# Kernel optimization log

Measured on AMD Instinct MI355X. Metric: run time of the kernel, lower is better.

The kernel has to match this reference:

```python
import jax, jax.numpy as jnp
import numpy as np

D_IN, N_HEADS, N_KV, HEAD_DIM = 2048, 8, 4, 256
GROUP = N_HEADS // N_KV
SCALING = 256.0 ** -0.5  # query_pre_attn_scalar = 256
EPS = 1e-6


def _rms_norm(x, gamma):
    # Gemma-style RMSNorm with (1 + gamma) scale, over last dim (head_dim)
    var = jnp.mean(x * x, axis=-1, keepdims=True)
    return x * jax.lax.rsqrt(var + EPS) * (1.0 + gamma)


def _apply_rope(x, cos, sin):
    # x: [b, h, s, d]; cos/sin: [s, d] (rotate-half convention)
    d = x.shape[-1]
    x1, x2 = x[..., : d // 2], x[..., d // 2:]
    rotated = jnp.concatenate([-x2, x1], axis=-1)
    return x * cos[None, None] + rotated * sin[None, None]


def setup_inputs() -> dict:
    key = jax.random.key(0)
    ks = jax.random.split(key, 6)
    b, s = 2, 2048
    x = jax.random.normal(ks[0], (b, s, D_IN), dtype=jnp.float32)
    # causal mask: True above diagonal = masked
    mask = jnp.triu(jnp.ones((s, s), dtype=bool), k=1)
    # RoPE tables (base 10000)
    inv_freq = 1.0 / (10000.0 ** (jnp.arange(0, HEAD_DIM, 2, dtype=jnp.float32) / HEAD_DIM))
    angles = jnp.arange(s, dtype=jnp.float32)[:, None] * inv_freq[None, :]  # [s, d/2]
    angles = jnp.concatenate([angles, angles], axis=-1)  # [s, d]
    cos, sin = jnp.cos(angles), jnp.sin(angles)
    std = 0.02
    wq = jax.random.normal(ks[1], (N_HEADS * HEAD_DIM, D_IN), dtype=jnp.float32) * std
    wk = jax.random.normal(ks[2], (N_KV * HEAD_DIM, D_IN), dtype=jnp.float32) * std
    wv = jax.random.normal(ks[3], (N_KV * HEAD_DIM, D_IN), dtype=jnp.float32) * std
    wo = jax.random.normal(ks[4], (D_IN, N_HEADS * HEAD_DIM), dtype=jnp.float32) * std
    q_gamma = jnp.zeros((HEAD_DIM,), dtype=jnp.float32)
    k_gamma = jnp.zeros((HEAD_DIM,), dtype=jnp.float32)
    return {"x": x, "mask": mask, "cos": cos, "sin": sin,
            "wq": wq, "wk": wk, "wv": wv, "wo": wo,
            "q_gamma": q_gamma, "k_gamma": k_gamma}


def reference(x, mask, cos, sin, wq, wk, wv, wo, q_gamma, k_gamma):
    b, s, _ = x.shape
    # projections (torch Linear: y = x @ W.T)
    q = (x @ wq.T).reshape(b, s, N_HEADS, HEAD_DIM).transpose(0, 2, 1, 3)  # [b,H,s,d]
    k = (x @ wk.T).reshape(b, s, N_KV, HEAD_DIM).transpose(0, 2, 1, 3)     # [b,G,s,d]
    v = (x @ wv.T).reshape(b, s, N_KV, HEAD_DIM).transpose(0, 2, 1, 3)     # [b,G,s,d]
    q = _rms_norm(q, q_gamma)
    k = _rms_norm(k, k_gamma)
    q = _apply_rope(q, cos, sin) * SCALING
    k = _apply_rope(k, cos, sin)
    # GQA via broadcast (avoids repeat_interleave): head h = g*GROUP + j (group-major)
    qg = q.reshape(b, N_KV, GROUP, s, HEAD_DIM)
    scores = jnp.einsum('bgjqd,bgkd->bgjqk', qg, k)  # [b,G,group,s,s]
    scores = jnp.where(mask[None, None, None], -jnp.inf, scores)
    weights = jax.nn.softmax(scores, axis=-1)
    ctx = jnp.einsum('bgjqk,bgkd->bgjqd', weights, v)  # [b,G,group,s,d]
    ctx = ctx.reshape(b, N_HEADS, s, HEAD_DIM).transpose(0, 2, 1, 3).reshape(b, s, N_HEADS * HEAD_DIM)
    return ctx @ wo.T
```

## Files before the change

### kernel.cpp

```cpp
#include <hip/hip_runtime.h>
#include <math.h>


typedef __bf16 bf16x8 __attribute__((ext_vector_type(8)));
typedef __bf16 bf16x4 __attribute__((ext_vector_type(4)));
typedef float  f32x4  __attribute__((ext_vector_type(4)));

#define MFMA16(a, b, c) __builtin_amdgcn_mfma_f32_16x16x32_bf16(a, b, c, 0, 0, 0)

__device__ __forceinline__ void async16(const __bf16* g, const __bf16* l) {
  __builtin_amdgcn_global_load_lds(
      (__attribute__((address_space(1))) const void*)g,
      (__attribute__((address_space(3))) void*)l, 16, 0, 0);
}

__global__ __launch_bounds__(256) void cast_f32_bf16(
    const float* __restrict__ src, __bf16* __restrict__ dst) {
  const size_t i = ((size_t)blockIdx.x * 256 + threadIdx.x) * 4;
  f32x4 v = *(const f32x4*)(src + i);
  bf16x4 o;
#pragma unroll
  for (int j = 0; j < 4; j++) o[j] = (__bf16)v[j];
  *(bf16x4*)(dst + i) = o;
}

template <typename OT>
__device__ __forceinline__ void gemm_body(const __bf16* A, const __bf16* B,
                                          OT* C, size_t m0, size_t n0,
                                          size_t ccol0, int ldc) {
  constexpr int K = 2048;
  __shared__ __align__(16) __bf16 As[128 * 32];
  __shared__ __align__(16) __bf16 Bs[128 * 32];
  const int tid = threadIdx.x;
  const int wave = tid >> 6, lane = tid & 63;
  const int lr = lane & 15, lq = lane >> 4;
  const int wm = (wave >> 1) * 64, wn = (wave & 1) * 64;

  f32x4 acc[4][4];
#pragma unroll
  for (int i = 0; i < 4; i++)
#pragma unroll
    for (int j = 0; j < 4; j++)
#pragma unroll
      for (int r = 0; r < 4; r++) acc[i][j][r] = 0.f;

  int srow[2], skof[2];
#pragma unroll
  for (int c = 0; c < 2; c++) {
    const int t = wave * 2 + c;
    const int g = t * 8 + (lane >> 3);
    const int cc = (lane & 7) ^ (g & 7);
    srow[c] = g * 2 + (cc >> 2);
    skof[c] = (cc & 3) * 8;
  }

  for (int k0 = 0; k0 < K; k0 += 32) {
#pragma unroll
    for (int c = 0; c < 2; c++) {
      const int t = wave * 2 + c;
      async16(A + (m0 + srow[c]) * K + k0 + skof[c], As + t * 512);
      async16(B + (n0 + srow[c]) * K + k0 + skof[c], Bs + t * 512);
    }
    __syncthreads();
    bf16x8 af[4], bf[4];
#pragma unroll
    for (int i = 0; i < 4; i++) {
      const int row = wm + i * 16 + lr;
      const int g = row >> 1;
      const int p = ((row & 1) * 4 + lq) ^ (g & 7);
      af[i] = *(const bf16x8*)&As[g * 64 + p * 8];
    }
#pragma unroll
    for (int j = 0; j < 4; j++) {
      const int row = wn + j * 16 + lr;
      const int g = row >> 1;
      const int p = ((row & 1) * 4 + lq) ^ (g & 7);
      bf[j] = *(const bf16x8*)&Bs[g * 64 + p * 8];
    }
#pragma unroll
    for (int i = 0; i < 4; i++)
#pragma unroll
      for (int j = 0; j < 4; j++)
        acc[i][j] = MFMA16(af[i], bf[j], acc[i][j]);
    __syncthreads();
  }

#pragma unroll
  for (int i = 0; i < 4; i++)
#pragma unroll
    for (int j = 0; j < 4; j++)
#pragma unroll
      for (int r = 0; r < 4; r++) {
        const size_t row = m0 + wm + i * 16 + lq * 4 + r;
        const size_t col = ccol0 + wn + j * 16 + lr;
        C[row * (size_t)ldc + col] = (OT)acc[i][j][r];
      }
}

template <typename OT>
__global__ __launch_bounds__(256) void gemm_bt(
    const __bf16* __restrict__ A, const __bf16* __restrict__ B,
    OT* __restrict__ C, const int ldc) {
  gemm_body<OT>(A, B, C, (size_t)blockIdx.y * 128, (size_t)blockIdx.x * 128,
                (size_t)blockIdx.x * 128, ldc);
}

__global__ __launch_bounds__(256) void gemm_qkv(
    const __bf16* __restrict__ A, const __bf16* __restrict__ Bq,
    const __bf16* __restrict__ Bk, const __bf16* __restrict__ Bv,
    __bf16* __restrict__ C) {
  const int bx = blockIdx.x;
  const __bf16* B;
  int nl;
  if (bx < 16) { B = Bq; nl = bx; }
  else if (bx < 24) { B = Bk; nl = bx - 16; }
  else { B = Bv; nl = bx - 24; }
  gemm_body<__bf16>(A, B, C, (size_t)blockIdx.y * 128, (size_t)nl * 128,
                    (size_t)bx * 128, 4096);
}

__global__ __launch_bounds__(256) void rmsrope(
    const __bf16* __restrict__ qkv, const float* __restrict__ cosb,
    const float* __restrict__ sinb, const float* __restrict__ qg,
    const float* __restrict__ kg, __bf16* __restrict__ qrot,
    __bf16* __restrict__ krot) {
  const int wave = threadIdx.x >> 6, lane = threadIdx.x & 63;
  const int rid = blockIdx.x * 4 + wave;
  const int m = rid / 12, seg = rid % 12;
  const int b = m >> 11, pos = m & 2047;
  const bool isq = seg < 8;
  const int col = isq ? seg * 256 : 2048 + (seg - 8) * 256;
  const int d = lane * 4;

  bf16x4 xv = *(const bf16x4*)(qkv + (size_t)m * 4096 + col + d);
  float x[4];
#pragma unroll
  for (int i = 0; i < 4; i++) x[i] = (float)xv[i];
  float ss = x[0] * x[0] + x[1] * x[1] + x[2] * x[2] + x[3] * x[3];
#pragma unroll
  for (int off = 1; off < 64; off <<= 1) ss += __shfl_xor(ss, off);
  const float inv = rsqrtf(ss * (1.f / 256.f) + 1e-6f);

  f32x4 gv = *(const f32x4*)((isq ? qg : kg) + d);
  float xn[4];
#pragma unroll
  for (int i = 0; i < 4; i++) xn[i] = x[i] * inv * (1.f + gv[i]);
  float rot[4];
#pragma unroll
  for (int i = 0; i < 4; i++) {
    const float pn = __shfl_xor(xn[i], 32);
    rot[i] = (lane < 32) ? -pn : pn;
  }
  f32x4 cv = *(const f32x4*)(cosb + (size_t)pos * 256 + d);
  f32x4 sv = *(const f32x4*)(sinb + (size_t)pos * 256 + d);
  const float sc = isq ? 0.0625f : 1.f;
  bf16x4 ov;
#pragma unroll
  for (int i = 0; i < 4; i++)
    ov[i] = (__bf16)((xn[i] * cv[i] + rot[i] * sv[i]) * sc);
  __bf16* dst = isq
      ? qrot + ((size_t)(b * 8 + seg) * 2048 + pos) * 256 + d
      : krot + ((size_t)(b * 4 + (seg - 8)) * 2048 + pos) * 256 + d;
  *(bf16x4*)dst = ov;
}

__global__ __launch_bounds__(256) void vtrans(const __bf16* __restrict__ qkv,
                                              __bf16* __restrict__ vT) {
  __shared__ __bf16 tile[64 * 65];
  const int bkv = blockIdx.z;
  const int d0 = blockIdx.y * 64, p0 = blockIdx.x * 64;
  const int t = threadIdx.x;
  const int b = bkv >> 2, kv = bkv & 3;
#pragma unroll
  for (int i = 0; i < 16; i++) {
    const int f = i * 256 + t;
    const int pl = f >> 6, dl = f & 63;
    tile[pl * 65 + dl] =
        qkv[(size_t)(b * 2048 + p0 + pl) * 4096 + 3072 + kv * 256 + d0 + dl];
  }
  __syncthreads();
#pragma unroll
  for (int i = 0; i < 16; i++) {
    const int f = i * 256 + t;
    const int dl = f >> 6, pl = f & 63;
    vT[((size_t)bkv * 256 + d0 + dl) * 2048 + p0 + pl] = tile[pl * 65 + dl];
  }
}

__global__ __launch_bounds__(128) void flash(
    const __bf16* __restrict__ qrot, const __bf16* __restrict__ krot,
    const __bf16* __restrict__ vT, __bf16* __restrict__ ctx) {
  __shared__ __align__(16) __bf16 Ks[64 * 256];
  __shared__ __align__(16) __bf16 Vs[256 * 64];
  __shared__ __align__(16) __bf16 Ps[2 * 32 * 64];
  const int tid = threadIdx.x, wave = tid >> 6, lane = tid & 63;
  const int lr = lane & 15, lq = lane >> 4;
  const int qt = (int)gridDim.x - 1 - (int)blockIdx.x;
  const int h = blockIdx.y, b = blockIdx.z, kv = h >> 1;
  const int q0 = qt * 64 + wave * 32;

  bf16x8 qf[2][8];
  {
    const __bf16* qbb = qrot + (size_t)(b * 8 + h) * 2048 * 256;
#pragma unroll
    for (int qi = 0; qi < 2; qi++)
#pragma unroll
      for (int i = 0; i < 8; i++)
        qf[qi][i] = *(const bf16x8*)(qbb + (size_t)(q0 + qi * 16 + lr) * 256 +
                                     i * 32 + lq * 8);
  }
  f32x4 acc[2][16];
#pragma unroll
  for (int qi = 0; qi < 2; qi++)
#pragma unroll
    for (int j = 0; j < 16; j++)
#pragma unroll
      for (int r = 0; r < 4; r++) acc[qi][j][r] = 0.f;
  float lsum[2][4];
#pragma unroll
  for (int qi = 0; qi < 2; qi++)
#pragma unroll
    for (int r = 0; r < 4; r++) lsum[qi][r] = 0.f;

  const __bf16* kbase = krot + (size_t)(b * 4 + kv) * 2048 * 256;
  const __bf16* vbase = vT + (size_t)(b * 4 + kv) * 256 * 2048;

  int koff[16], voff[16];
#pragma unroll
  for (int c = 0; c < 16; c++) {
    const int t = wave * 16 + c;
    {
      const int row = t * 2 + (lane >> 5);
      const int ch = (lane & 31) ^ (row & 31);
      koff[c] = row * 256 + ch * 8;
    }
    {
      const int d = t * 8 + (lane >> 3);
      const int ch = (lane & 7) ^ (d & 7);
      voff[c] = d * 2048 + ch * 8;
    }
  }

  for (int kt = 0; kt <= qt; kt++) {
    const int k0 = kt * 64;
#pragma unroll
    for (int c = 0; c < 16; c++) {
      const int t = wave * 16 + c;
      async16(kbase + (size_t)k0 * 256 + koff[c], Ks + t * 512);
      async16(vbase + k0 + voff[c], Vs + t * 512);
    }
    __syncthreads();

    f32x4 s[2][4];
#pragma unroll
    for (int qi = 0; qi < 2; qi++)
#pragma unroll
      for (int f = 0; f < 4; f++)
#pragma unroll
        for (int r = 0; r < 4; r++) s[qi][f][r] = 0.f;
#pragma unroll
    for (int i = 0; i < 8; i++) {
      bf16x8 kf[4];
#pragma unroll
      for (int f = 0; f < 4; f++) {
        const int row = f * 16 + lr;
        const int pch = (i * 4 + lq) ^ (row & 31);
        kf[f] = *(const bf16x8*)&Ks[row * 256 + pch * 8];
      }
#pragma unroll
      for (int qi = 0; qi < 2; qi++)
#pragma unroll
        for (int f = 0; f < 4; f++)
          s[qi][f] = MFMA16(qf[qi][i], kf[f], s[qi][f]);
    }

    const bool diag = (kt == qt);
#pragma unroll
    for (int qi = 0; qi < 2; qi++) {
      const int qa = q0 + qi * 16 + lq * 4;
#pragma unroll
      for (int f = 0; f < 4; f++) {
        const int ka = k0 + f * 16 + lr;
        const int row = qi * 16 + lq * 4;
        const int pchb = (f * 2 + (lr >> 3));
#pragma unroll
        for (int r = 0; r < 4; r++) {
          float p = __expf(s[qi][f][r] - 16.f);
          if (diag && ka > qa + r) p = 0.f;
          lsum[qi][r] += p;
          Ps[wave * 2048 + (row + r) * 64 + (pchb ^ ((row + r) & 7)) * 8 +
             (lr & 7)] = (__bf16)p;
        }
      }
    }
    asm volatile("s_waitcnt lgkmcnt(0)" ::: "memory");

#pragma unroll
    for (int m = 0; m < 2; m++) {
      bf16x8 pf[2];
#pragma unroll
      for (int qi = 0; qi < 2; qi++) {
        const int row = qi * 16 + lr;
        const int pch = (m * 4 + lq) ^ (row & 7);
        pf[qi] = *(const bf16x8*)&Ps[wave * 2048 + row * 64 + pch * 8];
      }
#pragma unroll
      for (int j = 0; j < 16; j++) {
        const int d = j * 16 + lr;
        const int pch = (m * 4 + lq) ^ (d & 7);
        bf16x8 vf = *(const bf16x8*)&Vs[d * 64 + pch * 8];
#pragma unroll
        for (int qi = 0; qi < 2; qi++)
          acc[qi][j] = MFMA16(pf[qi], vf, acc[qi][j]);
      }
    }
    __syncthreads();
  }

  float inv[2][4];
#pragma unroll
  for (int qi = 0; qi < 2; qi++)
#pragma unroll
    for (int r = 0; r < 4; r++) {
      float l = lsum[qi][r];
#pragma unroll
      for (int off = 1; off < 16; off <<= 1) l += __shfl_xor(l, off);
      inv[qi][r] = 1.f / l;
    }
#pragma unroll
  for (int qi = 0; qi < 2; qi++)
#pragma unroll
    for (int j = 0; j < 16; j++)
#pragma unroll
      for (int r = 0; r < 4; r++) {
        const int row = q0 + qi * 16 + lq * 4 + r;
        ctx[((size_t)(b * 2048 + row) * 8 + h) * 256 + j * 16 + lr] =
            (__bf16)(acc[qi][j][r] * inv[qi][r]);
      }
}

extern "C" void kernel_launch(void* const* d_in, const int* in_sizes, int n_in,
                              void* d_out, int out_size, void* d_ws,
                              size_t ws_size, hipStream_t stream) {
  const float* x = (const float*)d_in[0];
  const float* cosb = (const float*)d_in[2];
  const float* sinb = (const float*)d_in[3];
  const float* wq = (const float*)d_in[4];
  const float* wk = (const float*)d_in[5];
  const float* wv = (const float*)d_in[6];
  const float* wo = (const float*)d_in[7];
  const float* qg = (const float*)d_in[8];
  const float* kg = (const float*)d_in[9];
  float* out = (float*)d_out;

  char* ws = (char*)d_ws;
  __bf16* xbf = (__bf16*)ws;
  __bf16* wqbf = (__bf16*)(ws + ((size_t)16 << 20));
  __bf16* wkbf = (__bf16*)(ws + ((size_t)24 << 20));
  __bf16* wvbf = (__bf16*)(ws + ((size_t)28 << 20));
  __bf16* qkv = (__bf16*)(ws + ((size_t)32 << 20));
  __bf16* qrot = (__bf16*)ws;
  __bf16* krot = (__bf16*)(ws + ((size_t)16 << 20));
  __bf16* vTp = (__bf16*)(ws + ((size_t)24 << 20));
  __bf16* wobf = (__bf16*)(ws + ((size_t)32 << 20));
  __bf16* ctx = (__bf16*)(ws + ((size_t)40 << 20));

  cast_f32_bf16<<<8192, 256, 0, stream>>>(x, xbf);
  cast_f32_bf16<<<4096, 256, 0, stream>>>(wq, wqbf);
  cast_f32_bf16<<<2048, 256, 0, stream>>>(wk, wkbf);
  cast_f32_bf16<<<2048, 256, 0, stream>>>(wv, wvbf);

  gemm_qkv<<<dim3(32, 32), 256, 0, stream>>>(xbf, wqbf, wkbf, wvbf, qkv);

  rmsrope<<<12288, 256, 0, stream>>>(qkv, cosb, sinb, qg, kg, qrot, krot);
  vtrans<<<dim3(32, 4, 8), 256, 0, stream>>>(qkv, vTp);

  cast_f32_bf16<<<4096, 256, 0, stream>>>(wo, wobf);
  flash<<<dim3(32, 8, 2), 128, 0, stream>>>(qrot, krot, vTp, ctx);

  gemm_bt<float><<<dim3(16, 32), 256, 0, stream>>>(ctx, wobf, out, 2048);
}
```

Baseline: 425.2 us.

## Double-buffer K/V tiles in flash kernel and use 4-wave 128-query blocks

```diff
diff --git a/kernel.cpp b/kernel.cpp
--- a/kernel.cpp
+++ b/kernel.cpp
@@ -187,17 +187,17 @@
   }
 }
 
-__global__ __launch_bounds__(128) void flash(
+__global__ __launch_bounds__(256) void flash(
     const __bf16* __restrict__ qrot, const __bf16* __restrict__ krot,
     const __bf16* __restrict__ vT, __bf16* __restrict__ ctx) {
-  __shared__ __align__(16) __bf16 Ks[64 * 256];
-  __shared__ __align__(16) __bf16 Vs[256 * 64];
-  __shared__ __align__(16) __bf16 Ps[2 * 32 * 64];
+  __shared__ __align__(16) __bf16 Ks[2][64 * 256];
+  __shared__ __align__(16) __bf16 Vs[2][256 * 64];
+  __shared__ __align__(16) __bf16 Ps[4 * 32 * 64];
   const int tid = threadIdx.x, wave = tid >> 6, lane = tid & 63;
   const int lr = lane & 15, lq = lane >> 4;
-  const int qt = (int)gridDim.x - 1 - (int)blockIdx.x;
+  const int Q = blockIdx.x;
   const int h = blockIdx.y, b = blockIdx.z, kv = h >> 1;
-  const int q0 = qt * 64 + wave * 32;
+  const int q0 = Q * 128 + wave * 32;
 
   bf16x8 qf[2][8];
   {
@@ -225,10 +225,10 @@
   const __bf16* kbase = krot + (size_t)(b * 4 + kv) * 2048 * 256;
   const __bf16* vbase = vT + (size_t)(b * 4 + kv) * 256 * 2048;
 
-  int koff[16], voff[16];
-#pragma unroll
-  for (int c = 0; c < 16; c++) {
-    const int t = wave * 16 + c;
+  int koff[8], voff[8];
+#pragma unroll
+  for (int c = 0; c < 8; c++) {
+    const int t = wave * 8 + c;
     {
       const int row = t * 2 + (lane >> 5);
       const int ch = (lane & 31) ^ (row & 31);
@@ -241,15 +241,30 @@
     }
   }
 
-  for (int kt = 0; kt <= qt; kt++) {
+  const int nt = 2 * Q + 2;
+
+#define STAGE(kt_, buf_)                                                   \
+  {                                                                        \
+    const int k0_ = (kt_)*64;                                              \
+    _Pragma("unroll") for (int c = 0; c < 8; c++) {                        \
+      const int t = wave * 8 + c;                                          \
+      async16(kbase + (size_t)k0_ * 256 + koff[c], Ks[buf_] + t * 512);    \
+      async16(vbase + k0_ + voff[c], Vs[buf_] + t * 512);                  \
+    }                                                                      \
+  }
+
+  STAGE(0, 0);
+
+  for (int kt = 0; kt < nt; kt++) {
+    const int cur = kt & 1;
     const int k0 = kt * 64;
-#pragma unroll
-    for (int c = 0; c < 16; c++) {
-      const int t = wave * 16 + c;
-      async16(kbase + (size_t)k0 * 256 + koff[c], Ks + t * 512);
-      async16(vbase + k0 + voff[c], Vs + t * 512);
-    }
-    __syncthreads();
+    if (kt + 1 < nt) {
+      STAGE(kt + 1, cur ^ 1);
+      asm volatile("s_waitcnt vmcnt(16)" ::: "memory");
+    } else {
+      asm volatile("s_waitcnt vmcnt(0)" ::: "memory");
+    }
+    __builtin_amdgcn_s_barrier();
 
     f32x4 s[2][4];
 #pragma unroll
@@ -265,7 +280,7 @@
       for (int f = 0; f < 4; f++) {
         const int row = f * 16 + lr;
         const int pch = (i * 4 + lq) ^ (row & 31);
-        kf[f] = *(const bf16x8*)&Ks[row * 256 + pch * 8];
+        kf[f] = *(const bf16x8*)&Ks[cur][row * 256 + pch * 8];
       }
 #pragma unroll
       for (int qi = 0; qi < 2; qi++)
@@ -274,7 +289,7 @@
           s[qi][f] = MFMA16(qf[qi][i], kf[f], s[qi][f]);
     }
 
-    const bool diag = (kt == qt);
+    const bool diag = (k0 + 63 > q0);
 #pragma unroll
     for (int qi = 0; qi < 2; qi++) {
       const int qa = q0 + qi * 16 + lq * 4;
@@ -308,14 +323,15 @@
       for (int j = 0; j < 16; j++) {
         const int d = j * 16 + lr;
         const int pch = (m * 4 + lq) ^ (d & 7);
-        bf16x8 vf = *(const bf16x8*)&Vs[d * 64 + pch * 8];
+        bf16x8 vf = *(const bf16x8*)&Vs[cur][d * 64 + pch * 8];
 #pragma unroll
         for (int qi = 0; qi < 2; qi++)
           acc[qi][j] = MFMA16(pf[qi], vf, acc[qi][j]);
       }
     }
-    __syncthreads();
-  }
+    __builtin_amdgcn_s_barrier();
+  }
+#undef STAGE
 
   float inv[2][4];
 #pragma unroll
@@ -376,7 +392,7 @@
   vtrans<<<dim3(32, 4, 8), 256, 0, stream>>>(qkv, vTp);
 
   cast_f32_bf16<<<4096, 256, 0, stream>>>(wo, wobf);
-  flash<<<dim3(32, 8, 2), 128, 0, stream>>>(qrot, krot, vTp, ctx);
+  flash<<<dim3(16, 8, 2), 256, 0, stream>>>(qrot, krot, vTp, ctx);
 
   gemm_bt<float><<<dim3(16, 32), 256, 0, stream>>>(ctx, wobf, out, 2048);
 }
```

Result: no change. 425.8 us (+0.1%).

## Use 256x256-tile 8-wave QKV GEMM with double-buffered async LDS loads

Applied to the files above, without the earlier changes.

```diff
diff --git a/kernel.cpp b/kernel.cpp
--- a/kernel.cpp
+++ b/kernel.cpp
@@ -105,18 +105,109 @@
                 (size_t)blockIdx.x * 128, ldc);
 }
 
-__global__ __launch_bounds__(256) void gemm_qkv(
+__global__ __launch_bounds__(512, 2) void gemm_qkv8(
     const __bf16* __restrict__ A, const __bf16* __restrict__ Bq,
     const __bf16* __restrict__ Bk, const __bf16* __restrict__ Bv,
     __bf16* __restrict__ C) {
+  constexpr int NT = 32;
+  __shared__ __align__(16) __bf16 As[2][256 * 64];
+  __shared__ __align__(16) __bf16 Bs[2][256 * 64];
+
   const int bx = blockIdx.x;
-  const __bf16* B;
+  const __bf16* Bg;
   int nl;
-  if (bx < 16) { B = Bq; nl = bx; }
-  else if (bx < 24) { B = Bk; nl = bx - 16; }
-  else { B = Bv; nl = bx - 24; }
-  gemm_body<__bf16>(A, B, C, (size_t)blockIdx.y * 128, (size_t)nl * 128,
-                    (size_t)bx * 128, 4096);
+  if (bx < 8)       { Bg = Bq; nl = bx; }
+  else if (bx < 12) { Bg = Bk; nl = bx - 8; }
+  else              { Bg = Bv; nl = bx - 12; }
+  const size_t m0 = (size_t)blockIdx.y * 256;
+  const size_t n0 = (size_t)nl * 256;
+  const size_t ccol0 = (size_t)bx * 256;
+
+  const int tid = threadIdx.x;
+  const int wave = tid >> 6, lane = tid & 63;
+  const int lr = lane & 15, lq = lane >> 4;
+  const int wm = (wave >> 2) * 128, wn = (wave & 3) * 64;
+
+  f32x4 acc[8][4];
+#pragma unroll
+  for (int i = 0; i < 8; i++)
+#pragma unroll
+    for (int j = 0; j < 4; j++)
+#pragma unroll
+      for (int r = 0; r < 4; r++) acc[i][j][r] = 0.f;
+
+  const int srow0 = wave * 8 + (lane >> 3);
+  const int sc = ((lane & 7) ^ (srow0 & 7)) * 8;
+
+#define QSTAGE(kt_, nb_)                                                     \
+  {                                                                          \
+    const int k0_ = (kt_)*64;                                                \
+    _Pragma("unroll") for (int s = 0; s < 4; s++) {                          \
+      async16(A + (m0 + s * 64 + srow0) * 2048 + k0_ + sc,                   \
+              &As[nb_][s * 4096 + wave * 512]);                              \
+      async16(Bg + (n0 + s * 64 + srow0) * 2048 + k0_ + sc,                  \
+              &Bs[nb_][s * 4096 + wave * 512]);                              \
+    }                                                                        \
+  }
+
+  QSTAGE(0, 0);
+  __syncthreads();
+
+  for (int t = 0; t < NT; t++) {
+    const int nb = t & 1;
+    bf16x8 bf[8];
+#pragma unroll
+    for (int q = 0; q < 4; q++) {
+      bf16x8 af[4];
+#pragma unroll
+      for (int di = 0; di < 2; di++)
+#pragma unroll
+        for (int kk = 0; kk < 2; kk++) {
+          const int r = wm + q * 32 + di * 16 + lr;
+          af[di * 2 + kk] =
+              *(const bf16x8*)&As[nb][r * 64 + (((kk * 4 + lq) ^ (r & 7)) * 8)];
+        }
+      if (q == 0) {
+#pragma unroll
+        for (int nj = 0; nj < 4; nj++)
+#pragma unroll
+          for (int kk = 0; kk < 2; kk++) {
+            const int r = wn + nj * 16 + lr;
+            bf[nj * 2 + kk] = *(const bf16x8*)&Bs[nb][r * 64 +
+                                (((kk * 4 + lq) ^ (r & 7)) * 8)];
+          }
+        if (t + 1 < NT) QSTAGE(t + 1, nb ^ 1);
+      }
+      __builtin_amdgcn_s_barrier();
+      asm volatile("s_waitcnt lgkmcnt(0)" ::: "memory");
+      __builtin_amdgcn_sched_barrier(0);
+      __builtin_amdgcn_s_setprio(1);
+#pragma unroll
+      for (int di = 0; di < 2; di++)
+#pragma unroll
+        for (int nj = 0; nj < 4; nj++)
+#pragma unroll
+          for (int kk = 0; kk < 2; kk++)
+            acc[q * 2 + di][nj] =
+                MFMA16(af[di * 2 + kk], bf[nj * 2 + kk], acc[q * 2 + di][nj]);
+      __builtin_amdgcn_s_setprio(0);
+      if (q == 3)
+        asm volatile("s_waitcnt vmcnt(0)" ::: "memory");
+      __builtin_amdgcn_s_barrier();
+    }
+  }
+#undef QSTAGE
+
+#pragma unroll
+  for (int i = 0; i < 8; i++)
+#pragma unroll
+    for (int j = 0; j < 4; j++)
+#pragma unroll
+      for (int r = 0; r < 4; r++) {
+        const size_t row = m0 + wm + i * 16 + lq * 4 + r;
+        const size_t col = ccol0 + wn + j * 16 + lr;
+        C[row * 4096 + col] = (__bf16)acc[i][j][r];
+      }
 }
 
 __global__ __launch_bounds__(256) void rmsrope(
@@ -370,7 +461,7 @@
   cast_f32_bf16<<<2048, 256, 0, stream>>>(wk, wkbf);
   cast_f32_bf16<<<2048, 256, 0, stream>>>(wv, wvbf);
 
-  gemm_qkv<<<dim3(32, 32), 256, 0, stream>>>(xbf, wqbf, wkbf, wvbf, qkv);
+  gemm_qkv8<<<dim3(16, 16), 512, 0, stream>>>(xbf, wqbf, wkbf, wvbf, qkv);
 
   rmsrope<<<12288, 256, 0, stream>>>(qkv, cosb, sinb, qg, kg, qrot, krot);
   vtrans<<<dim3(32, 4, 8), 256, 0, stream>>>(qkv, vTp);
```

Result: faster. 405.0 us (-4.8%).
